# Optimization experiments

Measured on AMD Instinct MI355X. Metric: run time of the kernel, lower is better.

## Reference

```python
import math
import jax, jax.numpy as jnp
import numpy as np

B, S, D, H, DK = 2, 2048, 1024, 16, 64
NUM_BUCKETS, MAX_DISTANCE = 32, 128


def _relative_position_bucket(rel_pos):
    # bidirectional=True (encoder): is_decoder=False
    nb = NUM_BUCKETS // 2
    rel_buckets = (rel_pos > 0).astype(jnp.int32) * nb
    rp = jnp.abs(rel_pos)
    max_exact = nb // 2
    is_small = rp < max_exact
    rp_large = max_exact + (
        jnp.log(rp.astype(jnp.float32) / max_exact)
        / math.log(MAX_DISTANCE / max_exact)
        * (nb - max_exact)
    ).astype(jnp.int32)
    rp_large = jnp.minimum(rp_large, nb - 1)
    return rel_buckets + jnp.where(is_small, rp, rp_large)


def compute_bias(rel_bias, q_len, k_len):
    ctx = jnp.arange(q_len, dtype=jnp.int32)[:, None]
    mem = jnp.arange(k_len, dtype=jnp.int32)[None, :]
    buckets = _relative_position_bucket(mem - ctx)          # [q,k]
    vals = rel_bias[buckets]                                 # [q,k,H]
    return jnp.transpose(vals, (2, 0, 1))[None]              # [1,H,q,k]


def setup_inputs() -> dict:
    key = jax.random.key(0)
    ks = jax.random.split(key, 6)
    scale = 0.02
    return {
        "hidden_states": jax.random.normal(ks[0], (B, S, D), jnp.float32),
        "Wq": jax.random.normal(ks[1], (D, H * DK), jnp.float32) * scale,
        "Wk": jax.random.normal(ks[2], (D, H * DK), jnp.float32) * scale,
        "Wv": jax.random.normal(ks[3], (D, H * DK), jnp.float32) * scale,
        "Wo": jax.random.normal(ks[4], (H * DK, D), jnp.float32) * scale,
        "rel_bias": jax.random.normal(ks[5], (NUM_BUCKETS, H), jnp.float32) * scale,
    }


def reference(hidden_states, Wq, Wk, Wv, Wo, rel_bias):
    b, s, _ = hidden_states.shape

    def shape(x):  # [b,s,H*DK] -> [b,H,s,DK]
        return x.reshape(b, s, H, DK).transpose(0, 2, 1, 3)

    q = shape(hidden_states @ Wq)
    k = shape(hidden_states @ Wk)
    v = shape(hidden_states @ Wv)

    # T5: no 1/sqrt(d_k) scaling
    scores = jnp.einsum("bhqd,bhkd->bhqk", q, k)
    position_bias = compute_bias(rel_bias, s, s)             # [1,H,s,s]
    scores = scores + position_bias
    attn = jax.nn.softmax(scores.astype(jnp.float32), axis=-1).astype(scores.dtype)
    out = jnp.einsum("bhqk,bhkd->bhqd", attn, v)
    out = out.transpose(0, 2, 1, 3).reshape(b, s, H * DK)
    return out @ Wo
```

## Files before the change

### kernel.cpp

```cpp
#include <hip/hip_runtime.h>

#define HH 16
#define DKK 64
#define SS 2048
#define BB 2
#define DD 1024

typedef __attribute__((ext_vector_type(4))) float f32x4;
typedef __attribute__((ext_vector_type(8))) short bf16x8;
typedef __attribute__((ext_vector_type(4))) short s16x4;
typedef __attribute__((ext_vector_type(2))) int i32x2;

__device__ __forceinline__ short bf16b(float f) {
    union { float f; unsigned u; } x; x.f = f;
    unsigned r = (x.u + 0x7fffu + ((x.u >> 16) & 1u)) >> 16;
    return (short)r;
}

__device__ __forceinline__ unsigned f2u(float f) {
    union { float f; unsigned u; } x; x.f = f;
    return x.u;
}

__device__ __forceinline__ f32x4 mfma16(bf16x8 a, bf16x8 b, f32x4 c) {
    return __builtin_amdgcn_mfma_f32_16x16x32_bf16(a, b, c, 0, 0, 0);
}

__device__ __forceinline__ void lds16(const short* g, short* l) {
    __builtin_amdgcn_global_load_lds(
        (const __attribute__((address_space(1))) void*)g,
        (__attribute__((address_space(3))) void*)l, 16, 0, 0);
}

__global__ __launch_bounds__(256) void cvt_bf16(const float* __restrict__ x,
                                                short* __restrict__ y, int n) {
    int i = (blockIdx.x * 256 + threadIdx.x) * 4;
    if (i >= n) return;
    f32x4 v = *(const f32x4*)(x + i);
    s16x4 o;
    o.x = bf16b(v.x); o.y = bf16b(v.y); o.z = bf16b(v.z); o.w = bf16b(v.w);
    *(s16x4*)(y + i) = o;
}

__global__ __launch_bounds__(256) void transpose_w(
    const float* __restrict__ W0, const float* __restrict__ W1,
    const float* __restrict__ W2, const float* __restrict__ W3,
    short* __restrict__ T0, short* __restrict__ T1,
    short* __restrict__ T2, short* __restrict__ T3) {
    const float* W; short* T;
    switch (blockIdx.z) {
        case 0: W = W0; T = T0; break;
        case 1: W = W1; T = T1; break;
        case 2: W = W2; T = T2; break;
        default: W = W3; T = T3; break;
    }
    __shared__ short tile[32][33];
    int n0 = blockIdx.x * 32, k0 = blockIdx.y * 32;
    int tx = threadIdx.x & 31;
    int ty = (threadIdx.x >> 5) * 4;
#pragma unroll
    for (int i = 0; i < 4; i++)
        tile[ty + i][tx] = bf16b(W[(k0 + ty + i) * DD + n0 + tx]);
    __syncthreads();
#pragma unroll
    for (int i = 0; i < 4; i++)
        T[(n0 + ty + i) * DD + k0 + tx] = tile[tx][ty + i];
}

__global__ __launch_bounds__(256) void build_bias(const float* __restrict__ rb,
                                                  float* __restrict__ tab) {
    int idx = blockIdx.x * 256 + threadIdx.x;
    if (idx >= HH * 4095) return;
    int h = idx / 4095, d = idx % 4095;
    int rel = d - 2047;
    int bucket = (rel > 0) ? 16 : 0;
    unsigned r = (rel < 0) ? (unsigned)(-rel) : (unsigned)rel;
    int add;
    if (r < 8) add = (int)r;
    else {
        int e = 31 - __clz(r);
        unsigned long long r2 = (unsigned long long)r * (unsigned long long)r;
        int f = 2 * e + ((r2 >= (2ull << (2 * e))) ? 1 : 0);
        add = 8 + (f - 6);
        if (add > 15) add = 15;
    }
    bucket += add;
    tab[h * 4095 + d] = rb[bucket * HH + h] * 1.44269504f;
}

template <int EPI>
__global__ __launch_bounds__(256) void gemm_bt(
    const short* __restrict__ A,
    const short* __restrict__ Bq, const short* __restrict__ Bk, const short* __restrict__ Bv,
    short* __restrict__ Cq, short* __restrict__ Ck, short* __restrict__ Cvt,
    float* __restrict__ Cout) {
    const int K = 1024, N = 1024;
    __shared__ short As[128 * 32];
    __shared__ short Bs[128 * 32];
    int tid = threadIdx.x;
    int wave = tid >> 6, lane = tid & 63;
    int quad = lane >> 4, l16 = lane & 15;
    int m0 = blockIdx.y * 128, n0 = blockIdx.x * 128;
    const short* Bt = Bq;
    if (EPI == 0) { if (blockIdx.z == 1) Bt = Bk; else if (blockIdx.z == 2) Bt = Bv; }

    int wm = (wave & 1) * 64, wn = (wave >> 1) * 64;
    int r0 = tid >> 2, c0 = (tid & 3) * 8;

    f32x4 acc[4][4];
#pragma unroll
    for (int i = 0; i < 4; i++)
#pragma unroll
        for (int j = 0; j < 4; j++) acc[i][j] = (f32x4){0.f, 0.f, 0.f, 0.f};

    for (int k0 = 0; k0 < K; k0 += 32) {
        __syncthreads();
        lds16(A + (size_t)(m0 + r0) * K + k0 + c0, As + wave * 512);
        lds16(A + (size_t)(m0 + 64 + r0) * K + k0 + c0, As + 2048 + wave * 512);
        lds16(Bt + (size_t)(n0 + r0) * K + k0 + c0, Bs + wave * 512);
        lds16(Bt + (size_t)(n0 + 64 + r0) * K + k0 + c0, Bs + 2048 + wave * 512);
        __syncthreads();
        bf16x8 af[4], bfr[4];
#pragma unroll
        for (int t = 0; t < 4; t++) {
            af[t] = *(const bf16x8*)(As + (wm + t * 16 + l16) * 32 + quad * 8);
            bfr[t] = *(const bf16x8*)(Bs + (wn + t * 16 + l16) * 32 + quad * 8);
        }
#pragma unroll
        for (int mt = 0; mt < 4; mt++)
#pragma unroll
            for (int nt = 0; nt < 4; nt++)
                acc[mt][nt] = mfma16(af[mt], bfr[nt], acc[mt][nt]);
    }

#pragma unroll
    for (int mt = 0; mt < 4; mt++) {
#pragma unroll
        for (int nt = 0; nt < 4; nt++) {
#pragma unroll
            for (int r = 0; r < 4; r++) {
                int gm = m0 + wm + mt * 16 + quad * 4 + r;
                int gn = n0 + wn + nt * 16 + l16;
                float v = acc[mt][nt][r];
                if (EPI == 1) {
                    Cout[(size_t)gm * N + gn] = v;
                } else {
                    int b = gm >> 11, s = gm & 2047;
                    int h = gn >> 6, dk = gn & 63;
                    short bv = bf16b(v);
                    if (blockIdx.z == 0)
                        Cq[(((size_t)(b * HH + h)) * SS + s) * DKK + dk] = bv;
                    else if (blockIdx.z == 1)
                        Ck[(((size_t)(b * HH + h)) * SS + s) * DKK + dk] = bv;
                    else
                        Cvt[(((size_t)(b * HH + h)) * DKK + dk) * SS + s] = bv;
                }
            }
        }
    }
}

__global__ __launch_bounds__(256, 2) void attn(
    const short* __restrict__ Q, const short* __restrict__ Kmat,
    const short* __restrict__ Vt, const float* __restrict__ btab,
    short* __restrict__ O) {
    __shared__ short Ks[2][64 * 64];
    __shared__ short Vs[2][64 * 64];
    __shared__ float bias_s[2176];
    __shared__ short P_s[4][16 * 64];

    int tid = threadIdx.x;
    int wave = tid >> 6, lane = tid & 63;
    int quad = lane >> 4, l16 = lane & 15;
    int bh = blockIdx.x;
    int h = bh & 15, b = bh >> 4;
    int q0b = blockIdx.y * 128;
    int q0w = q0b + wave * 32;

    const short* Qb = Q + (size_t)bh * SS * DKK;
    const short* Kb = Kmat + (size_t)bh * SS * DKK;
    const short* Vb = Vt + (size_t)bh * DKK * SS;
    const float* bt = btab + h * 4095;

    int woff = 1920 - q0b;
    for (int i = tid; i < 2176; i += 256) {
        int gi = woff + i;
        bias_s[i] = bt[gi > 4094 ? 4094 : gi];
    }
    float blo = bt[2047 - 128];
    float bhi = bt[2047 + 128];

    int kro = tid >> 3;
    int gk = (tid & 7) ^ (kro & 7);
    const short* Kg0 = Kb + (size_t)kro * DKK + gk * 8;
    const short* Kg1 = Kb + (size_t)(kro + 32) * DKK + gk * 8;
    const short* Vg0 = Vb + (size_t)kro * SS + gk * 8;
    const short* Vg1 = Vb + (size_t)(kro + 32) * SS + gk * 8;

    bf16x8 qf[2][2];
#pragma unroll
    for (int qs = 0; qs < 2; qs++) {
        qf[qs][0] = *(const bf16x8*)(Qb + (q0w + qs * 16 + l16) * DKK + quad * 8);
        qf[qs][1] = *(const bf16x8*)(Qb + (q0w + qs * 16 + l16) * DKK + 32 + quad * 8);
    }

    f32x4 o[2][4];
#pragma unroll
    for (int qs = 0; qs < 2; qs++)
#pragma unroll
        for (int i = 0; i < 4; i++) o[qs][i] = (f32x4){0.f, 0.f, 0.f, 0.f};
    f32x4 lacc[2];
    lacc[0] = (f32x4){0.f, 0.f, 0.f, 0.f};
    lacc[1] = (f32x4){0.f, 0.f, 0.f, 0.f};

    bf16x8 onesf;
    short onev = (l16 == 0) ? (short)0x3F80 : (short)0;
#pragma unroll
    for (int i = 0; i < 8; i++) onesf[i] = onev;

    short* Pw = &P_s[wave][0];
    int gxor = l16 & 7;
    int ghalf = quad >> 1;
    int wbase = l16 * 64 + (quad & 1) * 4;
    int ra0 = l16 * 64 + ((quad ^ gxor) * 8);
    int ra1 = l16 * 64 + (((4 + quad) ^ gxor) * 8);
    int bidx = 127 + quad * 4 - wave * 32 - l16;
    int sl0 = (quad ^ gxor) * 8;
    int sl1 = ((4 + quad) ^ gxor) * 8;

    lds16(Kg0, &Ks[0][wave * 512]);
    lds16(Kg1, &Ks[0][2048 + wave * 512]);
    lds16(Vg0, &Vs[0][wave * 512]);
    lds16(Vg1, &Vs[0][2048 + wave * 512]);

    int cur = 0;
    for (int kc = 0; kc < SS; kc += 64) {
        __syncthreads();
        int kn = (kc + 64) & (SS - 1);
        int nxt = cur ^ 1;
        lds16(Kg0 + (size_t)kn * DKK, &Ks[nxt][wave * 512]);
        lds16(Kg1 + (size_t)kn * DKK, &Ks[nxt][2048 + wave * 512]);
        lds16(Vg0 + kn, &Vs[nxt][wave * 512]);
        lds16(Vg1 + kn, &Vs[nxt][2048 + wave * 512]);

        const short* Ksc = &Ks[cur][0];
        const short* Vsc = &Vs[cur][0];

        f32x4 s[2][4];
#pragma unroll
        for (int kt = 0; kt < 4; kt++) {
            int row = (kt * 16 + l16) * 64;
            bf16x8 kf0 = *(const bf16x8*)(Ksc + row + sl0);
            bf16x8 kf1 = *(const bf16x8*)(Ksc + row + sl1);
            s[0][kt] = mfma16(kf0, qf[0][0], (f32x4){0.f, 0.f, 0.f, 0.f});
            s[0][kt] = mfma16(kf1, qf[0][1], s[0][kt]);
            s[1][kt] = mfma16(kf0, qf[1][0], (f32x4){0.f, 0.f, 0.f, 0.f});
            s[1][kt] = mfma16(kf1, qf[1][1], s[1][kt]);
        }
        bf16x8 vf[4][2];
#pragma unroll
        for (int nt = 0; nt < 4; nt++) {
            int row = (nt * 16 + l16) * 64;
            vf[nt][0] = *(const bf16x8*)(Vsc + row + sl0);
            vf[nt][1] = *(const bf16x8*)(Vsc + row + sl1);
        }

#pragma unroll
        for (int qs = 0; qs < 2; qs++) {
            int q0s = q0w + qs * 16;
            bool nearb = (kc > q0s - 191) && (kc < q0s + 143);
            float bconst = (kc <= q0s - 191) ? blo : bhi;
#pragma unroll
            for (int kt = 0; kt < 4; kt++) {
                unsigned u[4];
#pragma unroll
                for (int r = 0; r < 4; r++) {
                    float bv = nearb ? bias_s[bidx + kc + kt * 16 + r - qs * 16]
                                     : bconst;
                    float p = __builtin_amdgcn_exp2f(
                        fmaf(s[qs][kt][r], 1.44269504f, bv));
                    u[r] = f2u(p) + 0x8000u;
                }
                unsigned d0 = __builtin_amdgcn_perm(u[1], u[0], 0x07060302u);
                unsigned d1 = __builtin_amdgcn_perm(u[3], u[2], 0x07060302u);
                int g = (kt * 2 + ghalf) ^ gxor;
                *(i32x2*)(Pw + wbase + g * 8) = (i32x2){(int)d0, (int)d1};
            }
            __asm__ __volatile__("" ::: "memory");
            bf16x8 pf0 = *(const bf16x8*)(Pw + ra0);
            bf16x8 pf1 = *(const bf16x8*)(Pw + ra1);
            lacc[qs] = mfma16(pf0, onesf, lacc[qs]);
            lacc[qs] = mfma16(pf1, onesf, lacc[qs]);
#pragma unroll
            for (int nt = 0; nt < 4; nt++) {
                o[qs][nt] = mfma16(pf0, vf[nt][0], o[qs][nt]);
                o[qs][nt] = mfma16(pf1, vf[nt][1], o[qs][nt]);
            }
            __asm__ __volatile__("" ::: "memory");
        }
        cur ^= 1;
    }

#pragma unroll
    for (int qs = 0; qs < 2; qs++) {
        float inv[4];
#pragma unroll
        for (int r = 0; r < 4; r++) {
            float l = __shfl(lacc[qs][r], lane & 48);
            inv[r] = 1.f / l;
        }
#pragma unroll
        for (int nt = 0; nt < 4; nt++)
#pragma unroll
            for (int r = 0; r < 4; r++) {
                int qrow = q0w + qs * 16 + quad * 4 + r;
                int dk = nt * 16 + l16;
                O[((size_t)(b * SS + qrow)) * (HH * DKK) + h * DKK + dk] =
                    bf16b(o[qs][nt][r] * inv[r]);
            }
    }
}

extern "C" void kernel_launch(void* const* d_in, const int* in_sizes, int n_in,
                              void* d_out, int out_size, void* d_ws, size_t ws_size,
                              hipStream_t stream) {
    const float* hs = (const float*)d_in[0];
    const float* Wq = (const float*)d_in[1];
    const float* Wk = (const float*)d_in[2];
    const float* Wv = (const float*)d_in[3];
    const float* Wo = (const float*)d_in[4];
    const float* rb = (const float*)d_in[5];
    float* out = (float*)d_out;

    char* ws = (char*)d_ws;
    size_t off = 0;
    auto alloc = [&](size_t bytes) -> void* {
        void* p = (void*)(ws + off);
        off += (bytes + 255) & ~(size_t)255;
        return p;
    };
    const size_t M = (size_t)BB * SS;
    short* hsb = (short*)alloc(M * DD * 2);
    short* WqT = (short*)alloc((size_t)DD * DD * 2);
    short* WkT = (short*)alloc((size_t)DD * DD * 2);
    short* WvT = (short*)alloc((size_t)DD * DD * 2);
    short* WoT = (short*)alloc((size_t)DD * DD * 2);
    short* Qb  = (short*)alloc(M * DD * 2);
    short* Kb  = (short*)alloc(M * DD * 2);
    short* VTb = (short*)alloc(M * DD * 2);
    short* Ab  = (short*)alloc(M * DD * 2);
    float* btab = (float*)alloc((size_t)HH * 4095 * 4);

    int nHS = (int)(M * DD);
    cvt_bf16<<<nHS / 1024, 256, 0, stream>>>(hs, hsb, nHS);
    transpose_w<<<dim3(32, 32, 4), 256, 0, stream>>>(Wq, Wk, Wv, Wo, WqT, WkT, WvT, WoT);
    build_bias<<<(HH * 4095 + 255) / 256, 256, 0, stream>>>(rb, btab);
    gemm_bt<0><<<dim3(8, 32, 3), 256, 0, stream>>>(hsb, WqT, WkT, WvT, Qb, Kb, VTb, nullptr);
    attn<<<dim3(32, 16), 256, 0, stream>>>(Qb, Kb, VTb, btab, Ab);
    gemm_bt<1><<<dim3(8, 32, 1), 256, 0, stream>>>(Ab, WoT, nullptr, nullptr,
                                                   nullptr, nullptr, nullptr, out);
}
```

Measured before the change: 222.5 us.

## Split GEMMs into fused QKV and smaller-tile output kernels; batch attention P stores

Replaces the templated GEMM with two kernels. gemm_qkv treats the three projection weights as one N=3072 matrix and picks the Q/K/V destination from the column index. gemm_out uses 64x128 tiles, doubling the block count for the output projection to fill more compute units. In attention, bias values are loaded into registers up front, and P is written for both query sub-tiles before a single barrier and the MFMAs, so LDS traffic and fences are batched. This costs more registers and LDS, and assumes the Q/K/V transposed weights sit contiguously in memory.

```diff
diff --git a/kernel.cpp b/kernel.cpp
--- a/kernel.cpp
+++ b/kernel.cpp
@@ -88,21 +88,16 @@
     tab[h * 4095 + d] = rb[bucket * HH + h] * 1.44269504f;
 }
 
-template <int EPI>
-__global__ __launch_bounds__(256) void gemm_bt(
-    const short* __restrict__ A,
-    const short* __restrict__ Bq, const short* __restrict__ Bk, const short* __restrict__ Bv,
-    short* __restrict__ Cq, short* __restrict__ Ck, short* __restrict__ Cvt,
-    float* __restrict__ Cout) {
-    const int K = 1024, N = 1024;
+__global__ __launch_bounds__(256) void gemm_qkv(
+    const short* __restrict__ A, const short* __restrict__ Wt,
+    short* __restrict__ Cq, short* __restrict__ Ck, short* __restrict__ Cvt) {
+    const int K = 1024;
     __shared__ short As[128 * 32];
     __shared__ short Bs[128 * 32];
     int tid = threadIdx.x;
     int wave = tid >> 6, lane = tid & 63;
     int quad = lane >> 4, l16 = lane & 15;
     int m0 = blockIdx.y * 128, n0 = blockIdx.x * 128;
-    const short* Bt = Bq;
-    if (EPI == 0) { if (blockIdx.z == 1) Bt = Bk; else if (blockIdx.z == 2) Bt = Bv; }
 
     int wm = (wave & 1) * 64, wn = (wave >> 1) * 64;
     int r0 = tid >> 2, c0 = (tid & 3) * 8;
@@ -117,8 +112,8 @@
         __syncthreads();
         lds16(A + (size_t)(m0 + r0) * K + k0 + c0, As + wave * 512);
         lds16(A + (size_t)(m0 + 64 + r0) * K + k0 + c0, As + 2048 + wave * 512);
-        lds16(Bt + (size_t)(n0 + r0) * K + k0 + c0, Bs + wave * 512);
-        lds16(Bt + (size_t)(n0 + 64 + r0) * K + k0 + c0, Bs + 2048 + wave * 512);
+        lds16(Wt + (size_t)(n0 + r0) * K + k0 + c0, Bs + wave * 512);
+        lds16(Wt + (size_t)(n0 + 64 + r0) * K + k0 + c0, Bs + 2048 + wave * 512);
         __syncthreads();
         bf16x8 af[4], bfr[4];
 #pragma unroll
@@ -141,23 +136,71 @@
             for (int r = 0; r < 4; r++) {
                 int gm = m0 + wm + mt * 16 + quad * 4 + r;
                 int gn = n0 + wn + nt * 16 + l16;
-                float v = acc[mt][nt][r];
-                if (EPI == 1) {
-                    Cout[(size_t)gm * N + gn] = v;
-                } else {
-                    int b = gm >> 11, s = gm & 2047;
-                    int h = gn >> 6, dk = gn & 63;
-                    short bv = bf16b(v);
-                    if (blockIdx.z == 0)
-                        Cq[(((size_t)(b * HH + h)) * SS + s) * DKK + dk] = bv;
-                    else if (blockIdx.z == 1)
-                        Ck[(((size_t)(b * HH + h)) * SS + s) * DKK + dk] = bv;
-                    else
-                        Cvt[(((size_t)(b * HH + h)) * DKK + dk) * SS + s] = bv;
-                }
-            }
-        }
-    }
+                int b = gm >> 11, s = gm & 2047;
+                int which = gn >> 10;
+                int h = (gn >> 6) & 15, dk = gn & 63;
+                short bv = bf16b(acc[mt][nt][r]);
+                if (which == 0)
+                    Cq[(((size_t)(b * HH + h)) * SS + s) * DKK + dk] = bv;
+                else if (which == 1)
+                    Ck[(((size_t)(b * HH + h)) * SS + s) * DKK + dk] = bv;
+                else
+                    Cvt[(((size_t)(b * HH + h)) * DKK + dk) * SS + s] = bv;
+            }
+        }
+    }
+}
+
+__global__ __launch_bounds__(256) void gemm_out(
+    const short* __restrict__ A, const short* __restrict__ Wt,
+    float* __restrict__ Cout) {
+    const int K = 1024, N = 1024;
+    __shared__ short As[64 * 32];
+    __shared__ short Bs[128 * 32];
+    int tid = threadIdx.x;
+    int wave = tid >> 6, lane = tid & 63;
+    int quad = lane >> 4, l16 = lane & 15;
+    int m0 = blockIdx.y * 64, n0 = blockIdx.x * 128;
+
+    int wm = (wave & 1) * 32, wn = (wave >> 1) * 64;
+    int r0 = tid >> 2, c0 = (tid & 3) * 8;
+
+    f32x4 acc[2][4];
+#pragma unroll
+    for (int i = 0; i < 2; i++)
+#pragma unroll
+        for (int j = 0; j < 4; j++) acc[i][j] = (f32x4){0.f, 0.f, 0.f, 0.f};
+
+    for (int k0 = 0; k0 < K; k0 += 32) {
+        __syncthreads();
+        lds16(A + (size_t)(m0 + r0) * K + k0 + c0, As + wave * 512);
+        lds16(Wt + (size_t)(n0 + r0) * K + k0 + c0, Bs + wave * 512);
+        lds16(Wt + (size_t)(n0 + 64 + r0) * K + k0 + c0, Bs + 2048 + wave * 512);
+        __syncthreads();
+        bf16x8 af[2], bfr[4];
+#pragma unroll
+        for (int t = 0; t < 2; t++)
+            af[t] = *(const bf16x8*)(As + (wm + t * 16 + l16) * 32 + quad * 8);
+#pragma unroll
+        for (int t = 0; t < 4; t++)
+            bfr[t] = *(const bf16x8*)(Bs + (wn + t * 16 + l16) * 32 + quad * 8);
+#pragma unroll
+        for (int mt = 0; mt < 2; mt++)
+#pragma unroll
+            for (int nt = 0; nt < 4; nt++)
+                acc[mt][nt] = mfma16(af[mt], bfr[nt], acc[mt][nt]);
+    }
+
+#pragma unroll
+    for (int mt = 0; mt < 2; mt++)
+#pragma unroll
+        for (int nt = 0; nt < 4; nt++)
+#pragma unroll
+            for (int r = 0; r < 4; r++) {
+                int gm = m0 + wm + mt * 16 + quad * 4 + r;
+                int gn = n0 + wn + nt * 16 + l16;
+                Cout[(size_t)gm * N + gn] = acc[mt][nt][r];
+            }
 }
 
 __global__ __launch_bounds__(256, 2) void attn(
@@ -167,7 +210,7 @@
     __shared__ short Ks[2][64 * 64];
     __shared__ short Vs[2][64 * 64];
     __shared__ float bias_s[2176];
-    __shared__ short P_s[4][16 * 64];
+    __shared__ short P_s[4][2][16 * 64];
 
     int tid = threadIdx.x;
     int wave = tid >> 6, lane = tid & 63;
@@ -218,7 +261,7 @@
 #pragma unroll
     for (int i = 0; i < 8; i++) onesf[i] = onev;
 
-    short* Pw = &P_s[wave][0];
+    short* Pw = &P_s[wave][0][0];
     int gxor = l16 & 7;
     int ghalf = quad >> 1;
     int wbase = l16 * 64 + (quad & 1) * 4;
@@ -243,6 +286,24 @@
         lds16(Vg0 + kn, &Vs[nxt][wave * 512]);
         lds16(Vg1 + kn, &Vs[nxt][2048 + wave * 512]);
 
+        float breg[2][16];
+#pragma unroll
+        for (int qs = 0; qs < 2; qs++) {
+            int q0s = q0w + qs * 16;
+            if (kc > q0s - 191 && kc < q0s + 143) {
+#pragma unroll
+                for (int kt = 0; kt < 4; kt++)
+#pragma unroll
+                    for (int r = 0; r < 4; r++)
+                        breg[qs][kt * 4 + r] =
+                            bias_s[bidx + kc + kt * 16 + r - qs * 16];
+            } else {
+                float bc = (kc <= q0s - 191) ? blo : bhi;
+#pragma unroll
+                for (int i = 0; i < 16; i++) breg[qs][i] = bc;
+            }
+        }
+
         const short* Ksc = &Ks[cur][0];
         const short* Vsc = &Vs[cur][0];
 
@@ -267,28 +328,26 @@
 
 #pragma unroll
         for (int qs = 0; qs < 2; qs++) {
-            int q0s = q0w + qs * 16;
-            bool nearb = (kc > q0s - 191) && (kc < q0s + 143);
-            float bconst = (kc <= q0s - 191) ? blo : bhi;
 #pragma unroll
             for (int kt = 0; kt < 4; kt++) {
                 unsigned u[4];
 #pragma unroll
                 for (int r = 0; r < 4; r++) {
-                    float bv = nearb ? bias_s[bidx + kc + kt * 16 + r - qs * 16]
-                                     : bconst;
                     float p = __builtin_amdgcn_exp2f(
-                        fmaf(s[qs][kt][r], 1.44269504f, bv));
+                        fmaf(s[qs][kt][r], 1.44269504f, breg[qs][kt * 4 + r]));
                     u[r] = f2u(p) + 0x8000u;
                 }
                 unsigned d0 = __builtin_amdgcn_perm(u[1], u[0], 0x07060302u);
                 unsigned d1 = __builtin_amdgcn_perm(u[3], u[2], 0x07060302u);
                 int g = (kt * 2 + ghalf) ^ gxor;
-                *(i32x2*)(Pw + wbase + g * 8) = (i32x2){(int)d0, (int)d1};
-            }
-            __asm__ __volatile__("" ::: "memory");
-            bf16x8 pf0 = *(const bf16x8*)(Pw + ra0);
-            bf16x8 pf1 = *(const bf16x8*)(Pw + ra1);
+                *(i32x2*)(Pw + qs * 1024 + wbase + g * 8) = (i32x2){(int)d0, (int)d1};
+            }
+        }
+        __asm__ __volatile__("" ::: "memory");
+#pragma unroll
+        for (int qs = 0; qs < 2; qs++) {
+            bf16x8 pf0 = *(const bf16x8*)(Pw + qs * 1024 + ra0);
+            bf16x8 pf1 = *(const bf16x8*)(Pw + qs * 1024 + ra1);
             lacc[qs] = mfma16(pf0, onesf, lacc[qs]);
             lacc[qs] = mfma16(pf1, onesf, lacc[qs]);
 #pragma unroll
@@ -296,8 +355,8 @@
                 o[qs][nt] = mfma16(pf0, vf[nt][0], o[qs][nt]);
                 o[qs][nt] = mfma16(pf1, vf[nt][1], o[qs][nt]);
             }
-            __asm__ __volatile__("" ::: "memory");
-        }
+        }
+        __asm__ __volatile__("" ::: "memory");
         cur ^= 1;
     }
 
@@ -355,8 +414,7 @@
     cvt_bf16<<<nHS / 1024, 256, 0, stream>>>(hs, hsb, nHS);
     transpose_w<<<dim3(32, 32, 4), 256, 0, stream>>>(Wq, Wk, Wv, Wo, WqT, WkT, WvT, WoT);
     build_bias<<<(HH * 4095 + 255) / 256, 256, 0, stream>>>(rb, btab);
-    gemm_bt<0><<<dim3(8, 32, 3), 256, 0, stream>>>(hsb, WqT, WkT, WvT, Qb, Kb, VTb, nullptr);
+    gemm_qkv<<<dim3(24, 32), 256, 0, stream>>>(hsb, WqT, Qb, Kb, VTb);
     attn<<<dim3(32, 16), 256, 0, stream>>>(Qb, Kb, VTb, btab, Ab);
-    gemm_bt<1><<<dim3(8, 32, 1), 256, 0, stream>>>(Ab, WoT, nullptr, nullptr,
-                                                   nullptr, nullptr, nullptr, out);
-}
+    gemm_out<<<dim3(8, 64), 256, 0, stream>>>(Ab, WoT, out);
+}
```

Result: faster. 196.3 us (-11.8%).
